# Optimization experiments

Hardware: AMD Instinct MI355X
Metric: run time of the kernel (lower is better)

The kernel has to match this reference:

```python
import jax, jax.numpy as jnp
import numpy as np

T, H, F, E = 1024, 2048, 4096, 8


def setup_inputs() -> dict:
    key = jax.random.key(0)
    ks = jax.random.split(key, 5)
    s = 0.02
    return {
        "x": jax.random.normal(ks[0], (1, 1, T, H), dtype=jnp.float32),
        "w_gate": jax.random.normal(ks[1], (H, E), dtype=jnp.float32) * s,
        "w1": jax.random.normal(ks[2], (E, H, F), dtype=jnp.float32) * s,
        "w3": jax.random.normal(ks[3], (E, H, F), dtype=jnp.float32) * s,
        "w2": jax.random.normal(ks[4], (E, F, H), dtype=jnp.float32) * s,
    }


def _top2_weights(logits):
    # Faithful to top_2(): emulated top-2 via max/eq/mask, then 2-way softmax
    # w0 = 1/(1+exp(ex1-ex0)) for the top-1 expert, 1-w0 for the top-2 expert.
    neg_min = jnp.finfo(logits.dtype).min
    ex0 = jnp.max(logits, axis=-1, keepdims=True)            # (1,1,T,1)
    cond0 = (logits == ex0)                                   # top-1 indicator (1,1,T,E)
    masked = jnp.where(cond0, neg_min, logits)
    ex1 = jnp.max(masked, axis=-1, keepdims=True)            # second max
    cond1 = (masked == ex1)                                   # top-2 indicator
    w0 = 1.0 / (1.0 + jnp.exp(ex1 - ex0))                    # sigmoid(ex0-ex1)
    c0 = cond0.astype(logits.dtype)
    c1 = cond1.astype(logits.dtype)
    # c0*w0 - c1*(w0-1) == c0*w0 + c1*(1-w0)
    return c0 * w0 - c1 * (w0 - 1.0)                         # (1,1,T,E)


def reference(x, w_gate, w1, w3, w2):
    # x: (1,1,T,H)
    logits = jnp.einsum("abth,he->abte", x, w_gate)          # gate (1,1,T,E)
    weights = _top2_weights(logits)                           # (1,1,T,E)
    # SwiGLU experts, all experts on all tokens (dense, as in per-device replica)
    h1 = jnp.einsum("abth,ehf->eabtf", x, w1)
    h3 = jnp.einsum("abth,ehf->eabtf", x, w3)
    y = jnp.einsum("eabtf,efh->eabth", jax.nn.silu(h1) * h3, w2)
    # per-expert scale then sum over experts (= all-gather + reduce-mask matmul)
    out = jnp.einsum("eabth,abte->abth", y, weights)
    return out
```

## Files before the change

### kernel.cpp

```cpp
#include <hip/hip_runtime.h>
#include <hip/hip_bf16.h>

#define T_DIM 1024
#define H_DIM 2048
#define F_DIM 4096
#define E_DIM 8

typedef unsigned short u16;
typedef unsigned int u32;
typedef __attribute__((ext_vector_type(8))) short bf16x8;
typedef __attribute__((ext_vector_type(4))) float f32x4;

__device__ __forceinline__ u16 f2bf(float f) {
  u32 u = __builtin_bit_cast(u32, f);
  u32 r = (u + 0x7fffu + ((u >> 16) & 1u)) >> 16;
  return (u16)r;
}

__global__ __launch_bounds__(256) void gate_cvt_kernel(
    const float* __restrict__ x, const float* __restrict__ wg,
    u16* __restrict__ xb, float* __restrict__ wts) {
  int wave = threadIdx.x >> 6;
  int lane = threadIdx.x & 63;
  int t = blockIdx.x * 4 + wave;
  const float4* x4 = reinterpret_cast<const float4*>(x) + (size_t)t * 512;
  ushort4* xb4 = reinterpret_cast<ushort4*>(xb) + (size_t)t * 512;
  const float4* wg4 = reinterpret_cast<const float4*>(wg);

  float acc[8];
#pragma unroll
  for (int e = 0; e < 8; e++) acc[e] = 0.f;

#pragma unroll
  for (int i = 0; i < 8; i++) {
    int idx = i * 64 + lane;
    float4 v = x4[idx];
    ushort4 o = {f2bf(v.x), f2bf(v.y), f2bf(v.z), f2bf(v.w)};
    xb4[idx] = o;
    float xs[4] = {v.x, v.y, v.z, v.w};
    int hbase = idx * 4;
#pragma unroll
    for (int j = 0; j < 4; j++) {
      float4 wa = wg4[(hbase + j) * 2];
      float4 wb = wg4[(hbase + j) * 2 + 1];
      acc[0] += xs[j] * wa.x; acc[1] += xs[j] * wa.y;
      acc[2] += xs[j] * wa.z; acc[3] += xs[j] * wa.w;
      acc[4] += xs[j] * wb.x; acc[5] += xs[j] * wb.y;
      acc[6] += xs[j] * wb.z; acc[7] += xs[j] * wb.w;
    }
  }
#pragma unroll
  for (int e = 0; e < 8; e++) {
#pragma unroll
    for (int off = 32; off > 0; off >>= 1) acc[e] += __shfl_xor(acc[e], off, 64);
  }
  if (lane == 0) {
    const float NEG_MIN = -3.402823466e38f;
    float ex0 = acc[0];
#pragma unroll
    for (int e = 1; e < 8; e++) ex0 = fmaxf(ex0, acc[e]);
    float masked[8];
#pragma unroll
    for (int e = 0; e < 8; e++) masked[e] = (acc[e] == ex0) ? NEG_MIN : acc[e];
    float ex1 = masked[0];
#pragma unroll
    for (int e = 1; e < 8; e++) ex1 = fmaxf(ex1, masked[e]);
    float w0 = 1.f / (1.f + expf(ex1 - ex0));
#pragma unroll
    for (int e = 0; e < 8; e++) {
      float w = (acc[e] == ex0) ? w0 : ((masked[e] == ex1) ? (1.f - w0) : 0.f);
      wts[t * 8 + e] = w;
    }
  }
}

__global__ __launch_bounds__(512) void route_kernel(
    const float* __restrict__ wts, int* __restrict__ tlist,
    int* __restrict__ counts) {
  int e = threadIdx.x >> 6;
  int lane = threadIdx.x & 63;
  int base = 0;
  for (int c = 0; c < T_DIM; c += 64) {
    float w = wts[(c + lane) * 8 + e];
    unsigned long long m = __ballot(w != 0.f);
    if (w != 0.f) {
      int pos = base + __popcll(m & ((1ull << lane) - 1ull));
      tlist[e * T_DIM + pos] = c + lane;
    }
    base += __popcll(m);
  }
  if (lane == 0) counts[e] = base;
}

__global__ __launch_bounds__(256) void transpose_cvt_kernel(
    const float* __restrict__ src, u16* __restrict__ dst, int R, int C) {
  __shared__ u16 tile[64][68];
  long eoff = (long)blockIdx.z * R * C;
  const float* s = src + eoff;
  u16* d = dst + eoff;
  int c0 = blockIdx.x * 64, r0 = blockIdx.y * 64;
  int tid = threadIdx.x;
#pragma unroll
  for (int p = 0; p < 4; p++) {
    int idx = tid + p * 256;
    int r = idx >> 4, c4 = (idx & 15) << 2;
    float4 v = *reinterpret_cast<const float4*>(s + (long)(r0 + r) * C + c0 + c4);
    ushort4 o = {f2bf(v.x), f2bf(v.y), f2bf(v.z), f2bf(v.w)};
    *reinterpret_cast<ushort4*>(&tile[r][c4]) = o;
  }
  __syncthreads();
#pragma unroll
  for (int p = 0; p < 4; p++) {
    int idx = tid + p * 256;
    int c = idx >> 4, r4 = (idx & 15) << 2;
    ushort4 o = {tile[r4][c], tile[r4 + 1][c], tile[r4 + 2][c], tile[r4 + 3][c]};
    *reinterpret_cast<ushort4*>(d + (long)(c0 + c) * R + r0 + r4) = o;
  }
}

__global__ __launch_bounds__(256, 2) void h_kernel(
    const u16* __restrict__ xb, const u16* __restrict__ w1t,
    const u16* __restrict__ w3t, u16* __restrict__ hout,
    const int* __restrict__ tlist, const int* __restrict__ counts,
    int e_base) {
  int el = blockIdx.z;
  int eg = e_base + el;
  int ne = counts[eg];
  int t0 = blockIdx.y * 128;
  if (t0 >= ne) return;

  __shared__ u16 As[128 * 72];
  __shared__ u16 B1s[64 * 72];
  __shared__ u16 B3s[64 * 72];
  __shared__ int toks[128];

  int f0 = blockIdx.x * 64;
  const u16* b1 = w1t + (long)el * F_DIM * H_DIM;
  const u16* b3 = w3t + (long)el * F_DIM * H_DIM;
  int tid = threadIdx.x;
  if (tid < 128) {
    int i = t0 + tid;
    toks[tid] = tlist[eg * T_DIM + (i < ne ? i : ne - 1)];
  }
  __syncthreads();

  int wave = tid >> 6, lane = tid & 63;
  int wm = wave >> 1, wn = wave & 1;
  int mrow = lane & 15, quad = lane >> 4;

  const u16* aptr[4];
  int aoff[4];
#pragma unroll
  for (int it = 0; it < 4; it++) {
    int chunk = tid + it * 256;
    int r = chunk >> 3, c8 = (chunk & 7) << 3;
    aptr[it] = xb + (long)toks[r] * H_DIM + c8;
    aoff[it] = r * 72 + c8;
  }

  f32x4 acc1[4][2], acc3[4][2];
#pragma unroll
  for (int mt = 0; mt < 4; mt++)
#pragma unroll
    for (int nt = 0; nt < 2; nt++) { acc1[mt][nt] = (f32x4)(0.f); acc3[mt][nt] = (f32x4)(0.f); }

  for (int kt = 0; kt < H_DIM; kt += 64) {
#pragma unroll
    for (int it = 0; it < 4; it++) {
      uint4 v = *reinterpret_cast<const uint4*>(aptr[it] + kt);
      *reinterpret_cast<uint4*>(&As[aoff[it]]) = v;
    }
#pragma unroll
    for (int it = 0; it < 2; it++) {
      int chunk = tid + it * 256;
      int r = chunk >> 3, c8 = (chunk & 7) << 3;
      long off = (long)(f0 + r) * H_DIM + kt + c8;
      uint4 v1 = *reinterpret_cast<const uint4*>(b1 + off);
      uint4 v3 = *reinterpret_cast<const uint4*>(b3 + off);
      *reinterpret_cast<uint4*>(&B1s[r * 72 + c8]) = v1;
      *reinterpret_cast<uint4*>(&B3s[r * 72 + c8]) = v3;
    }
    __syncthreads();
#pragma unroll
    for (int kh = 0; kh < 2; kh++) {
      int koff = kh * 32 + quad * 8;
      bf16x8 af[4], b1f[2], b3f[2];
#pragma unroll
      for (int mt = 0; mt < 4; mt++)
        af[mt] = *reinterpret_cast<const bf16x8*>(&As[(wm * 64 + mt * 16 + mrow) * 72 + koff]);
#pragma unroll
      for (int nt = 0; nt < 2; nt++) {
        b1f[nt] = *reinterpret_cast<const bf16x8*>(&B1s[(wn * 32 + nt * 16 + mrow) * 72 + koff]);
        b3f[nt] = *reinterpret_cast<const bf16x8*>(&B3s[(wn * 32 + nt * 16 + mrow) * 72 + koff]);
      }
#pragma unroll
      for (int mt = 0; mt < 4; mt++)
#pragma unroll
        for (int nt = 0; nt < 2; nt++) {
          acc1[mt][nt] = __builtin_amdgcn_mfma_f32_16x16x32_bf16(af[mt], b1f[nt], acc1[mt][nt], 0, 0, 0);
          acc3[mt][nt] = __builtin_amdgcn_mfma_f32_16x16x32_bf16(af[mt], b3f[nt], acc3[mt][nt], 0, 0, 0);
        }
    }
    __syncthreads();
  }
  u16* hp = hout + (long)el * T_DIM * F_DIM;
#pragma unroll
  for (int mt = 0; mt < 4; mt++) {
#pragma unroll
    for (int r = 0; r < 4; r++) {
      int row = t0 + wm * 64 + mt * 16 + quad * 4 + r;
      if (row < ne) {
#pragma unroll
        for (int nt = 0; nt < 2; nt++) {
          int col = f0 + wn * 32 + nt * 16 + mrow;
          float v1 = acc1[mt][nt][r];
          float v3 = acc3[mt][nt][r];
          float sw = (v1 / (1.f + expf(-v1))) * v3;
          hp[(long)row * F_DIM + col] = f2bf(sw);
        }
      }
    }
  }
}

__global__ __launch_bounds__(256, 2) void y_kernel(
    const u16* __restrict__ h, const u16* __restrict__ w2t,
    const float* __restrict__ wts, float* __restrict__ out,
    const int* __restrict__ tlist, const int* __restrict__ counts,
    int e_base) {
  int el = blockIdx.z;
  int eg = e_base + el;
  int ne = counts[eg];
  int t0 = blockIdx.y * 128;
  if (t0 >= ne) return;

  __shared__ u16 As[128 * 72];
  __shared__ u16 Bs[64 * 72];
  int n0 = blockIdx.x * 64;
  const u16* a = h + (long)el * T_DIM * F_DIM;
  const u16* b = w2t + (long)el * H_DIM * F_DIM;
  int tid = threadIdx.x;
  int wave = tid >> 6, lane = tid & 63;
  int wm = wave >> 1, wn = wave & 1;
  int mrow = lane & 15, quad = lane >> 4;

  f32x4 acc[4][2];
#pragma unroll
  for (int mt = 0; mt < 4; mt++)
#pragma unroll
    for (int nt = 0; nt < 2; nt++) acc[mt][nt] = (f32x4)(0.f);

  for (int kt = 0; kt < F_DIM; kt += 64) {
#pragma unroll
    for (int it = 0; it < 4; it++) {
      int chunk = tid + it * 256;
      int r = chunk >> 3, c8 = (chunk & 7) << 3;
      uint4 v = *reinterpret_cast<const uint4*>(a + (long)(t0 + r) * F_DIM + kt + c8);
      *reinterpret_cast<uint4*>(&As[r * 72 + c8]) = v;
    }
#pragma unroll
    for (int it = 0; it < 2; it++) {
      int chunk = tid + it * 256;
      int r = chunk >> 3, c8 = (chunk & 7) << 3;
      uint4 v = *reinterpret_cast<const uint4*>(b + (long)(n0 + r) * F_DIM + kt + c8);
      *reinterpret_cast<uint4*>(&Bs[r * 72 + c8]) = v;
    }
    __syncthreads();
#pragma unroll
    for (int kh = 0; kh < 2; kh++) {
      int koff = kh * 32 + quad * 8;
      bf16x8 af[4], bf[2];
#pragma unroll
      for (int mt = 0; mt < 4; mt++)
        af[mt] = *reinterpret_cast<const bf16x8*>(&As[(wm * 64 + mt * 16 + mrow) * 72 + koff]);
#pragma unroll
      for (int nt = 0; nt < 2; nt++)
        bf[nt] = *reinterpret_cast<const bf16x8*>(&Bs[(wn * 32 + nt * 16 + mrow) * 72 + koff]);
#pragma unroll
      for (int mt = 0; mt < 4; mt++)
#pragma unroll
        for (int nt = 0; nt < 2; nt++)
          acc[mt][nt] = __builtin_amdgcn_mfma_f32_16x16x32_bf16(af[mt], bf[nt], acc[mt][nt], 0, 0, 0);
    }
    __syncthreads();
  }
#pragma unroll
  for (int mt = 0; mt < 4; mt++) {
#pragma unroll
    for (int r = 0; r < 4; r++) {
      int row = t0 + wm * 64 + mt * 16 + quad * 4 + r;
      if (row < ne) {
        int tok = tlist[eg * T_DIM + row];
        float wt = wts[tok * 8 + eg];
#pragma unroll
        for (int nt = 0; nt < 2; nt++) {
          int col = n0 + wn * 32 + nt * 16 + mrow;
          unsafeAtomicAdd(&out[(long)tok * H_DIM + col], acc[mt][nt][r] * wt);
        }
      }
    }
  }
}

extern "C" void kernel_launch(void* const* d_in, const int* in_sizes, int n_in,
                              void* d_out, int out_size, void* d_ws, size_t ws_size,
                              hipStream_t stream) {
  const float* x  = (const float*)d_in[0];
  const float* wg = (const float*)d_in[1];
  const float* w1 = (const float*)d_in[2];
  const float* w3 = (const float*)d_in[3];
  const float* w2 = (const float*)d_in[4];
  float* out = (float*)d_out;

  char* p = (char*)d_ws;
  u16* xb = (u16*)p;            p += (size_t)T_DIM * H_DIM * 2;
  float* wts = (float*)p;       p += (size_t)T_DIM * E_DIM * 4;
  int* tlist = (int*)p;         p += (size_t)E_DIM * T_DIM * 4;
  int* counts = (int*)p;        p += 256;
  size_t fixed = (size_t)(p - (char*)d_ws);
  size_t perE = (size_t)F_DIM * H_DIM * 2 * 3 + (size_t)T_DIM * F_DIM * 2;
  int G = 1;
  for (int g = 8; g >= 1; g >>= 1) {
    if (fixed + (size_t)g * perE <= ws_size) { G = g; break; }
  }
  u16* w1t = (u16*)p;           p += (size_t)G * F_DIM * H_DIM * 2;
  u16* w3t = (u16*)p;           p += (size_t)G * F_DIM * H_DIM * 2;
  u16* w2t = (u16*)p;           p += (size_t)G * H_DIM * F_DIM * 2;
  u16* hbuf = (u16*)p;

  gate_cvt_kernel<<<T_DIM / 4, 256, 0, stream>>>(x, wg, xb, wts);
  route_kernel<<<1, 512, 0, stream>>>(wts, tlist, counts);
  hipMemsetAsync(d_out, 0, (size_t)out_size * 4, stream);

  for (int e0 = 0; e0 < E_DIM; e0 += G) {
    transpose_cvt_kernel<<<dim3(F_DIM / 64, H_DIM / 64, G), 256, 0, stream>>>(
        w1 + (size_t)e0 * H_DIM * F_DIM, w1t, H_DIM, F_DIM);
    transpose_cvt_kernel<<<dim3(F_DIM / 64, H_DIM / 64, G), 256, 0, stream>>>(
        w3 + (size_t)e0 * H_DIM * F_DIM, w3t, H_DIM, F_DIM);
    transpose_cvt_kernel<<<dim3(H_DIM / 64, F_DIM / 64, G), 256, 0, stream>>>(
        w2 + (size_t)e0 * F_DIM * H_DIM, w2t, F_DIM, H_DIM);
    h_kernel<<<dim3(F_DIM / 64, T_DIM / 128, G), 256, 0, stream>>>(
        xb, w1t, w3t, hbuf, tlist, counts, e0);
    y_kernel<<<dim3(H_DIM / 64, T_DIM / 128, G), 256, 0, stream>>>(
        hbuf, w2t, wts, out, tlist, counts, e0);
  }
}
```

Before: 1.016 ms.

## Fuse fp32 weight transpose and bf16 conversion into the GEMM tile loaders

```diff
diff --git a/kernel.cpp b/kernel.cpp
--- a/kernel.cpp
+++ b/kernel.cpp
@@ -92,40 +92,12 @@
   if (lane == 0) counts[e] = base;
 }
 
-__global__ __launch_bounds__(256) void transpose_cvt_kernel(
-    const float* __restrict__ src, u16* __restrict__ dst, int R, int C) {
-  __shared__ u16 tile[64][68];
-  long eoff = (long)blockIdx.z * R * C;
-  const float* s = src + eoff;
-  u16* d = dst + eoff;
-  int c0 = blockIdx.x * 64, r0 = blockIdx.y * 64;
-  int tid = threadIdx.x;
-#pragma unroll
-  for (int p = 0; p < 4; p++) {
-    int idx = tid + p * 256;
-    int r = idx >> 4, c4 = (idx & 15) << 2;
-    float4 v = *reinterpret_cast<const float4*>(s + (long)(r0 + r) * C + c0 + c4);
-    ushort4 o = {f2bf(v.x), f2bf(v.y), f2bf(v.z), f2bf(v.w)};
-    *reinterpret_cast<ushort4*>(&tile[r][c4]) = o;
-  }
-  __syncthreads();
-#pragma unroll
-  for (int p = 0; p < 4; p++) {
-    int idx = tid + p * 256;
-    int c = idx >> 4, r4 = (idx & 15) << 2;
-    ushort4 o = {tile[r4][c], tile[r4 + 1][c], tile[r4 + 2][c], tile[r4 + 3][c]};
-    *reinterpret_cast<ushort4*>(d + (long)(c0 + c) * R + r0 + r4) = o;
-  }
-}
-
 __global__ __launch_bounds__(256, 2) void h_kernel(
-    const u16* __restrict__ xb, const u16* __restrict__ w1t,
-    const u16* __restrict__ w3t, u16* __restrict__ hout,
-    const int* __restrict__ tlist, const int* __restrict__ counts,
-    int e_base) {
+    const u16* __restrict__ xb, const float* __restrict__ w1,
+    const float* __restrict__ w3, u16* __restrict__ hout,
+    const int* __restrict__ tlist, const int* __restrict__ counts) {
   int el = blockIdx.z;
-  int eg = e_base + el;
-  int ne = counts[eg];
+  int ne = counts[el];
   int t0 = blockIdx.y * 128;
   if (t0 >= ne) return;
 
@@ -135,12 +107,12 @@
   __shared__ int toks[128];
 
   int f0 = blockIdx.x * 64;
-  const u16* b1 = w1t + (long)el * F_DIM * H_DIM;
-  const u16* b3 = w3t + (long)el * F_DIM * H_DIM;
+  const float* b1 = w1 + (long)el * H_DIM * F_DIM;
+  const float* b3 = w3 + (long)el * H_DIM * F_DIM;
   int tid = threadIdx.x;
   if (tid < 128) {
     int i = t0 + tid;
-    toks[tid] = tlist[eg * T_DIM + (i < ne ? i : ne - 1)];
+    toks[tid] = tlist[el * T_DIM + (i < ne ? i : ne - 1)];
   }
   __syncthreads();
 
@@ -158,6 +130,32 @@
     aoff[it] = r * 72 + c8;
   }
 
+  int bf4 = (tid & 15) << 2;
+  int bk0 = (tid >> 4) << 2;
+  int bwoff[4];
+#pragma unroll
+  for (int j = 0; j < 4; j++) {
+    int f = bf4 + j;
+    bwoff[j] = f * 72 + (bk0 ^ (((f >> 2) & 7) << 3));
+  }
+  const float* gb1 = b1 + (long)bk0 * F_DIM + f0 + bf4;
+  const float* gb3 = b3 + (long)bk0 * F_DIM + f0 + bf4;
+
+  int aroff[4][2], broff[2][2];
+#pragma unroll
+  for (int mt = 0; mt < 4; mt++)
+#pragma unroll
+    for (int kh = 0; kh < 2; kh++)
+      aroff[mt][kh] = (wm * 64 + mt * 16 + mrow) * 72 + kh * 32 + quad * 8;
+#pragma unroll
+  for (int nt = 0; nt < 2; nt++) {
+    int row = wn * 32 + nt * 16 + mrow;
+    int sw = ((row >> 2) & 7) << 3;
+#pragma unroll
+    for (int kh = 0; kh < 2; kh++)
+      broff[nt][kh] = row * 72 + ((kh * 32 + quad * 8) ^ sw);
+  }
+
   f32x4 acc1[4][2], acc3[4][2];
 #pragma unroll
   for (int mt = 0; mt < 4; mt++)
@@ -170,28 +168,35 @@
       uint4 v = *reinterpret_cast<const uint4*>(aptr[it] + kt);
       *reinterpret_cast<uint4*>(&As[aoff[it]]) = v;
     }
-#pragma unroll
-    for (int it = 0; it < 2; it++) {
-      int chunk = tid + it * 256;
-      int r = chunk >> 3, c8 = (chunk & 7) << 3;
-      long off = (long)(f0 + r) * H_DIM + kt + c8;
-      uint4 v1 = *reinterpret_cast<const uint4*>(b1 + off);
-      uint4 v3 = *reinterpret_cast<const uint4*>(b3 + off);
-      *reinterpret_cast<uint4*>(&B1s[r * 72 + c8]) = v1;
-      *reinterpret_cast<uint4*>(&B3s[r * 72 + c8]) = v3;
+    float4 r1[4], r3[4];
+    const float* g1 = gb1 + (long)kt * F_DIM;
+    const float* g3 = gb3 + (long)kt * F_DIM;
+#pragma unroll
+    for (int kk = 0; kk < 4; kk++) {
+      r1[kk] = *reinterpret_cast<const float4*>(g1 + (long)kk * F_DIM);
+      r3[kk] = *reinterpret_cast<const float4*>(g3 + (long)kk * F_DIM);
+    }
+#pragma unroll
+    for (int j = 0; j < 4; j++) {
+      u32 lo1 = (u32)f2bf(((const float*)&r1[0])[j]) | ((u32)f2bf(((const float*)&r1[1])[j]) << 16);
+      u32 hi1 = (u32)f2bf(((const float*)&r1[2])[j]) | ((u32)f2bf(((const float*)&r1[3])[j]) << 16);
+      u32 lo3 = (u32)f2bf(((const float*)&r3[0])[j]) | ((u32)f2bf(((const float*)&r3[1])[j]) << 16);
+      u32 hi3 = (u32)f2bf(((const float*)&r3[2])[j]) | ((u32)f2bf(((const float*)&r3[3])[j]) << 16);
+      uint2 p1 = {lo1, hi1}, p3 = {lo3, hi3};
+      *reinterpret_cast<uint2*>(&B1s[bwoff[j]]) = p1;
+      *reinterpret_cast<uint2*>(&B3s[bwoff[j]]) = p3;
     }
     __syncthreads();
 #pragma unroll
     for (int kh = 0; kh < 2; kh++) {
-      int koff = kh * 32 + quad * 8;
       bf16x8 af[4], b1f[2], b3f[2];
 #pragma unroll
       for (int mt = 0; mt < 4; mt++)
-        af[mt] = *reinterpret_cast<const bf16x8*>(&As[(wm * 64 + mt * 16 + mrow) * 72 + koff]);
+        af[mt] = *reinterpret_cast<const bf16x8*>(&As[aroff[mt][kh]]);
 #pragma unroll
       for (int nt = 0; nt < 2; nt++) {
-        b1f[nt] = *reinterpret_cast<const bf16x8*>(&B1s[(wn * 32 + nt * 16 + mrow) * 72 + koff]);
-        b3f[nt] = *reinterpret_cast<const bf16x8*>(&B3s[(wn * 32 + nt * 16 + mrow) * 72 + koff]);
+        b1f[nt] = *reinterpret_cast<const bf16x8*>(&B1s[broff[nt][kh]]);
+        b3f[nt] = *reinterpret_cast<const bf16x8*>(&B3s[broff[nt][kh]]);
       }
 #pragma unroll
       for (int mt = 0; mt < 4; mt++)
@@ -224,13 +229,11 @@
 }
 
 __global__ __launch_bounds__(256, 2) void y_kernel(
-    const u16* __restrict__ h, const u16* __restrict__ w2t,
+    const u16* __restrict__ h, const float* __restrict__ w2,
     const float* __restrict__ wts, float* __restrict__ out,
-    const int* __restrict__ tlist, const int* __restrict__ counts,
-    int e_base) {
+    const int* __restrict__ tlist, const int* __restrict__ counts) {
   int el = blockIdx.z;
-  int eg = e_base + el;
-  int ne = counts[eg];
+  int ne = counts[el];
   int t0 = blockIdx.y * 128;
   if (t0 >= ne) return;
 
@@ -238,11 +241,36 @@
   __shared__ u16 Bs[64 * 72];
   int n0 = blockIdx.x * 64;
   const u16* a = h + (long)el * T_DIM * F_DIM;
-  const u16* b = w2t + (long)el * H_DIM * F_DIM;
+  const float* b = w2 + (long)el * F_DIM * H_DIM;
   int tid = threadIdx.x;
   int wave = tid >> 6, lane = tid & 63;
   int wm = wave >> 1, wn = wave & 1;
   int mrow = lane & 15, quad = lane >> 4;
+
+  int bh4 = (tid & 15) << 2;
+  int bk0 = (tid >> 4) << 2;
+  int bwoff[4];
+#pragma unroll
+  for (int j = 0; j < 4; j++) {
+    int f = bh4 + j;
+    bwoff[j] = f * 72 + (bk0 ^ (((f >> 2) & 7) << 3));
+  }
+  const float* gb = b + (long)bk0 * H_DIM + n0 + bh4;
+
+  int aroff[4][2], broff[2][2];
+#pragma unroll
+  for (int mt = 0; mt < 4; mt++)
+#pragma unroll
+    for (int kh = 0; kh < 2; kh++)
+      aroff[mt][kh] = (wm * 64 + mt * 16 + mrow) * 72 + kh * 32 + quad * 8;
+#pragma unroll
+  for (int nt = 0; nt < 2; nt++) {
+    int row = wn * 32 + nt * 16 + mrow;
+    int sw = ((row >> 2) & 7) << 3;
+#pragma unroll
+    for (int kh = 0; kh < 2; kh++)
+      broff[nt][kh] = row * 72 + ((kh * 32 + quad * 8) ^ sw);
+  }
 
   f32x4 acc[4][2];
 #pragma unroll
@@ -258,24 +286,28 @@
       uint4 v = *reinterpret_cast<const uint4*>(a + (long)(t0 + r) * F_DIM + kt + c8);
       *reinterpret_cast<uint4*>(&As[r * 72 + c8]) = v;
     }
-#pragma unroll
-    for (int it = 0; it < 2; it++) {
-      int chunk = tid + it * 256;
-      int r = chunk >> 3, c8 = (chunk & 7) << 3;
-      uint4 v = *reinterpret_cast<const uint4*>(b + (long)(n0 + r) * F_DIM + kt + c8);
-      *reinterpret_cast<uint4*>(&Bs[r * 72 + c8]) = v;
+    float4 rb[4];
+    const float* g = gb + (long)kt * H_DIM;
+#pragma unroll
+    for (int kk = 0; kk < 4; kk++)
+      rb[kk] = *reinterpret_cast<const float4*>(g + (long)kk * H_DIM);
+#pragma unroll
+    for (int j = 0; j < 4; j++) {
+      u32 lo = (u32)f2bf(((const float*)&rb[0])[j]) | ((u32)f2bf(((const float*)&rb[1])[j]) << 16);
+      u32 hi = (u32)f2bf(((const float*)&rb[2])[j]) | ((u32)f2bf(((const float*)&rb[3])[j]) << 16);
+      uint2 pb = {lo, hi};
+      *reinterpret_cast<uint2*>(&Bs[bwoff[j]]) = pb;
     }
     __syncthreads();
 #pragma unroll
     for (int kh = 0; kh < 2; kh++) {
-      int koff = kh * 32 + quad * 8;
       bf16x8 af[4], bf[2];
 #pragma unroll
       for (int mt = 0; mt < 4; mt++)
-        af[mt] = *reinterpret_cast<const bf16x8*>(&As[(wm * 64 + mt * 16 + mrow) * 72 + koff]);
+        af[mt] = *reinterpret_cast<const bf16x8*>(&As[aroff[mt][kh]]);
 #pragma unroll
       for (int nt = 0; nt < 2; nt++)
-        bf[nt] = *reinterpret_cast<const bf16x8*>(&Bs[(wn * 32 + nt * 16 + mrow) * 72 + koff]);
+        bf[nt] = *reinterpret_cast<const bf16x8*>(&Bs[broff[nt][kh]]);
 #pragma unroll
       for (int mt = 0; mt < 4; mt++)
 #pragma unroll
@@ -290,8 +322,8 @@
     for (int r = 0; r < 4; r++) {
       int row = t0 + wm * 64 + mt * 16 + quad * 4 + r;
       if (row < ne) {
-        int tok = tlist[eg * T_DIM + row];
-        float wt = wts[tok * 8 + eg];
+        int tok = tlist[el * T_DIM + row];
+        float wt = wts[tok * 8 + el];
 #pragma unroll
         for (int nt = 0; nt < 2; nt++) {
           int col = n0 + wn * 32 + nt * 16 + mrow;
@@ -317,31 +349,14 @@
   float* wts = (float*)p;       p += (size_t)T_DIM * E_DIM * 4;
   int* tlist = (int*)p;         p += (size_t)E_DIM * T_DIM * 4;
   int* counts = (int*)p;        p += 256;
-  size_t fixed = (size_t)(p - (char*)d_ws);
-  size_t perE = (size_t)F_DIM * H_DIM * 2 * 3 + (size_t)T_DIM * F_DIM * 2;
-  int G = 1;
-  for (int g = 8; g >= 1; g >>= 1) {
-    if (fixed + (size_t)g * perE <= ws_size) { G = g; break; }
-  }
-  u16* w1t = (u16*)p;           p += (size_t)G * F_DIM * H_DIM * 2;
-  u16* w3t = (u16*)p;           p += (size_t)G * F_DIM * H_DIM * 2;
-  u16* w2t = (u16*)p;           p += (size_t)G * H_DIM * F_DIM * 2;
   u16* hbuf = (u16*)p;
 
   gate_cvt_kernel<<<T_DIM / 4, 256, 0, stream>>>(x, wg, xb, wts);
   route_kernel<<<1, 512, 0, stream>>>(wts, tlist, counts);
   hipMemsetAsync(d_out, 0, (size_t)out_size * 4, stream);
 
-  for (int e0 = 0; e0 < E_DIM; e0 += G) {
-    transpose_cvt_kernel<<<dim3(F_DIM / 64, H_DIM / 64, G), 256, 0, stream>>>(
-        w1 + (size_t)e0 * H_DIM * F_DIM, w1t, H_DIM, F_DIM);
-    transpose_cvt_kernel<<<dim3(F_DIM / 64, H_DIM / 64, G), 256, 0, stream>>>(
-        w3 + (size_t)e0 * H_DIM * F_DIM, w3t, H_DIM, F_DIM);
-    transpose_cvt_kernel<<<dim3(H_DIM / 64, F_DIM / 64, G), 256, 0, stream>>>(
-        w2 + (size_t)e0 * F_DIM * H_DIM, w2t, F_DIM, H_DIM);
-    h_kernel<<<dim3(F_DIM / 64, T_DIM / 128, G), 256, 0, stream>>>(
-        xb, w1t, w3t, hbuf, tlist, counts, e0);
-    y_kernel<<<dim3(H_DIM / 64, T_DIM / 128, G), 256, 0, stream>>>(
-        hbuf, w2t, wts, out, tlist, counts, e0);
-  }
-}
+  h_kernel<<<dim3(F_DIM / 64, T_DIM / 128, E_DIM), 256, 0, stream>>>(
+      xb, w1, w3, hbuf, tlist, counts);
+  y_kernel<<<dim3(H_DIM / 64, T_DIM / 128, E_DIM), 256, 0, stream>>>(
+      hbuf, w2, wts, out, tlist, counts);
+}
```

Measured after the change: 900.9 us. 1.13x faster.
